# Kernel tuning notes

Measured on AMD Instinct MI355X. Metric: run time of the kernel, lower is better.

The kernel has to match this reference:

```python
import jax, jax.numpy as jnp
import numpy as np

# BatchIrregularDownsample2d(number_downsample=2) faithful JAX reference.
# The torch module does host-synced, per-batch mask-driven compaction with
# data-dependent slicing. Index arithmetic is done host-side with numpy on the
# concrete integer pooling_mask (it is a non-differentiable int constant, and the
# original module syncs it to host via .item() anyway); the heavy data movement
# (gather over [B,C,N]) is done in jnp.

D = 2                      # number_downsample
B, C, H, W = 8, 256, 256, 256
BLOCK = 2 ** D             # quadtree alignment block (4x4)


def _build_mask(seed=0):
    """Quadtree-valid mask [B,1,H,W]: each aligned 4x4 block has one level in {0,1,2};
    identical histogram per batch (static shapes), different spatial layout."""
    hb, wb = H // BLOCK, W // BLOCK
    n = hb * wb                                  # 4096 blocks
    counts = [n - 2 * (n // 3), n // 3, n // 3]  # [1366, 1365, 1365]
    base = np.repeat(np.arange(D + 1), counts)
    out = []
    for b in range(B):
        rng = np.random.RandomState(seed + b)
        v = base.copy()
        rng.shuffle(v)
        m = v.reshape(hb, wb).repeat(BLOCK, 0).repeat(BLOCK, 1)
        out.append(m)
    return np.stack(out)[:, None].astype(np.int32)


def _build_indices(mask_np):
    """Replicates the per-batch compaction of the torch module, returning a dense
    gather-index matrix G [B,M] into input's token dim and a validity mask V [B,M]
    (zeros emulate the original's zero padding to max_elements)."""
    Bm = mask_np.shape[0]
    s = 2 ** (D - 1)
    per_batch = []
    for b in range(Bm):
        m = mask_np[b, 0]
        start = 0
        for i in range(D - 1):                   # start_idx: higher-res prefix
            start += int((m == i).sum()) // 4 ** i
        cs = (m >= D - 1)[::s, ::s]              # current_scale_mask, subsampled
        dt = (m < D)[::s, ::s]                   # dont_touch_mask, subsampled
        r, c = np.nonzero(cs)                    # row-major, matches torch.nonzero
        topleft = ((r % 2) + (c % 2)) == 0       # top-left of each 2x2 pool window
        dt_at = dt[r, c]
        keep_lower = topleft & ~dt_at            # pooled-down representatives
        pos = np.arange(r.shape[0])              # rank inside graph_current_res
        idx_b = np.concatenate([
            np.arange(start),                    # graph_higher_res (untouched prefix)
            start + pos[dt_at],                  # output_dont_touch
            start + pos[keep_lower],             # output_lower_res
        ])
        per_batch.append(idx_b)
    M = max(len(x) for x in per_batch)           # max_elements across batch
    G = np.zeros((Bm, M), np.int32)
    V = np.zeros((Bm, M), np.float32)
    for b, idx_b in enumerate(per_batch):
        G[b, :len(idx_b)] = idx_b
        V[b, :len(idx_b)] = 1.0
    return jnp.asarray(G), jnp.asarray(V)


def setup_inputs() -> dict:
    mask_np = _build_mask()
    # N = max_b nr_valid_elements_current (tokens actually addressed by the slicing)
    N = 0
    for b in range(B):
        m = mask_np[b, 0]
        n = 0
        for i in range(D):
            n += int(((m == i) if i < D - 1 else (m >= i)).sum()) // 4 ** i
        N = max(N, n)
    key = jax.random.key(0)
    x = jax.random.normal(key, (B, C, N), dtype=jnp.float32)
    return {"input": x, "pooling_mask": jnp.asarray(mask_np)}


def reference(input, pooling_mask):
    G, V = _build_indices(np.asarray(pooling_mask))
    # one fused gather over the token dim + zero-padding via validity mask
    out = jnp.take_along_axis(input, G[:, None, :], axis=2) * V[:, None, :]
    return out
```

## Files before the change

kernel.cpp:

```cpp
#include <hip/hip_runtime.h>
#include <hip/hip_bf16.h>


#define HW_FULL 65536
#define T1     1024
#define PER_T  16
#define CS_CAP 11264
#define TB     512

typedef float f4a __attribute__((ext_vector_type(4), aligned(4)));
typedef float f4v __attribute__((ext_vector_type(4)));
typedef int   i4a __attribute__((ext_vector_type(4), aligned(4)));

__global__ __launch_bounds__(1024) void build_idx_kernel(
    const int* __restrict__ mask, int* __restrict__ hdr, int* __restrict__ gt, int M)
{
    const int b = blockIdx.x;
    const int t = threadIdx.x;
    const int* mb = mask + (long long)b * HW_FULL;

    unsigned char fl[PER_T];
    unsigned long long local = 0ULL;
    #pragma unroll
    for (int k = 0; k < PER_T; ++k) {
        int e = t * PER_T + k;
        int r = e >> 7;
        int c = e & 127;
        int m = mb[(r << 9) + (c << 1)];
        int z  = (m == 0);
        int cs = (m >= 1);
        int dt = (m == 1);
        int tl = ((r | c) & 1) == 0;
        int kl = (tl && (m >= 2)) ? 1 : 0;
        fl[k] = (unsigned char)(z | (cs << 1) | (dt << 2) | (kl << 3));
        local += (unsigned long long)z
               | ((unsigned long long)cs << 16)
               | ((unsigned long long)dt << 32)
               | ((unsigned long long)kl << 48);
    }

    __shared__ unsigned long long sh[T1];
    sh[t] = local;
    __syncthreads();
    for (int off = 1; off < T1; off <<= 1) {
        unsigned long long v = (t >= off) ? sh[t - off] : 0ULL;
        __syncthreads();
        sh[t] += v;
        __syncthreads();
    }
    unsigned long long tot = sh[T1 - 1];
    unsigned long long ex  = (t > 0) ? sh[t - 1] : 0ULL;

    const int zt    = (int)( tot        & 0xFFFF);
    const int cst   = (int)((tot >> 16) & 0xFFFF);
    const int ndt   = (int)((tot >> 32) & 0xFFFF);
    const int nkl   = (int)((tot >> 48) & 0xFFFF);
    const int start = zt * 4;

    int csP = (int)((ex >> 16) & 0xFFFF);
    int dtP = (int)((ex >> 32) & 0xFFFF);
    int klP = (int)((ex >> 48) & 0xFFFF);

    int* gtb = gt + (long long)b * M;
    #pragma unroll
    for (int k = 0; k < PER_T; ++k) {
        int f = fl[k];
        if (f & 4) { gtb[dtP]       = start + csP; ++dtP; }
        if (f & 8) { gtb[ndt + klP] = start + csP; ++klP; }
        if (f & 2) { ++csP; }
    }

    if (t == 0) {
        hdr[b * 4 + 0] = start;
        hdr[b * 4 + 1] = cst;
        hdr[b * 4 + 2] = ndt + nkl;
        hdr[b * 4 + 3] = start + ndt + nkl;
    }
}

__global__ __launch_bounds__(TB) void fused_row_kernel(
    const float* __restrict__ in, const int* __restrict__ hdr,
    const int* __restrict__ gt, float* __restrict__ out,
    int N, int M, int cshift)
{
    const int row   = blockIdx.x;
    const int b     = row >> cshift;
    const int start = hdr[b * 4 + 0];
    const int csn   = hdr[b * 4 + 1];
    const int ntail = hdr[b * 4 + 2];
    const long long rowM = (long long)row * M;
    const long long rowN = (long long)row * N;
    const int tid = threadIdx.x;

    const float* rin  = in  + rowN;
    const float* src  = rin + start;
    const int*   gtb  = gt + (long long)b * M;
    float*       rout = out + rowM;

    __shared__ __align__(16) float lds[CS_CAP];
    const bool staged = (csn <= CS_CAP);

    if (staged) {
        const int cs4 = csn & ~3;
        for (int i = tid << 2; i < cs4; i += (TB << 2)) {
            f4a lv = *reinterpret_cast<const f4a*>(src + i);
            f4v v; v.x = lv.x; v.y = lv.y; v.z = lv.z; v.w = lv.w;
            *reinterpret_cast<f4v*>(&lds[i]) = v;
        }
        if (tid < (csn & 3)) lds[(csn & ~3) + tid] = src[(csn & ~3) + tid];
    }

    const int h  = (int)((4 - (rowM & 3)) & 3);
    const int nq = (start >= h) ? ((start - h) >> 2) : 0;
    for (int k = tid; k < nq; k += TB) {
        const int j = h + (k << 2);
        f4a lv = *reinterpret_cast<const f4a*>(rin + j);
        f4v v; v.x = lv.x; v.y = lv.y; v.z = lv.z; v.w = lv.w;
        __builtin_nontemporal_store(v, reinterpret_cast<f4v*>(rout + j));
    }
    if (tid == 0) {
        const int hh = (h < start) ? h : start;
        for (int j = 0; j < hh; ++j)
            __builtin_nontemporal_store(rin[j], rout + j);
        if (start >= h) {
            const int base = h + (nq << 2);
            for (int j = base; j < start; ++j)
                __builtin_nontemporal_store(rin[j], rout + j);
        }
    }

    __syncthreads();

    const int span = M - start;
    const int h2   = (h < span) ? h : span;
    const int nq2  = (span >= h) ? ((span - h) >> 2) : 0;

    for (int k = tid; k < nq2; k += TB) {
        const int t = h + (k << 2);
        i4a g = *reinterpret_cast<const i4a*>(gtb + t);
        f4v v;
        v.x = (t + 0 < ntail) ? (staged ? lds[g.x - start] : rin[g.x]) : 0.0f;
        v.y = (t + 1 < ntail) ? (staged ? lds[g.y - start] : rin[g.y]) : 0.0f;
        v.z = (t + 2 < ntail) ? (staged ? lds[g.z - start] : rin[g.z]) : 0.0f;
        v.w = (t + 3 < ntail) ? (staged ? lds[g.w - start] : rin[g.w]) : 0.0f;
        __builtin_nontemporal_store(v, reinterpret_cast<f4v*>(rout + start + t));
    }
    if (tid == TB - 1) {
        for (int t = 0; t < h2; ++t) {
            float x = (t < ntail) ? (staged ? lds[gtb[t] - start] : rin[gtb[t]]) : 0.0f;
            __builtin_nontemporal_store(x, rout + start + t);
        }
        if (span >= h) {
            for (int t = h + (nq2 << 2); t < span; ++t) {
                float x = (t < ntail) ? (staged ? lds[gtb[t] - start] : rin[gtb[t]]) : 0.0f;
                __builtin_nontemporal_store(x, rout + start + t);
            }
        }
    }
}

extern "C" void kernel_launch(void* const* d_in, const int* in_sizes, int n_in,
                              void* d_out, int out_size, void* d_ws, size_t ws_size,
                              hipStream_t stream) {
    const float* x    = (const float*)d_in[0];
    const int*   mask = (const int*)d_in[1];
    float*       out  = (float*)d_out;

    const int B = in_sizes[1] / HW_FULL;
    const int C = 256;
    const int N = in_sizes[0] / (B * C);
    const int M = out_size   / (B * C);
    const int nrows = B * C;

    int cshift = 0;
    while ((1 << cshift) < C) ++cshift;

    int* hdr = (int*)d_ws;
    int* gt  = hdr + 32;

    build_idx_kernel<<<B, T1, 0, stream>>>(mask, hdr, gt, M);
    fused_row_kernel<<<nrows, TB, 0, stream>>>(x, hdr, gt, out, N, M, cshift);
}
```

Measured before the change: 101.0 us.

## Prefetch staging loads into registers and use wave-shuffle scan for index build

The index-build kernel now writes the per-element flags to shared memory with coalesced mask reads, then replaces the 1024-step shared-memory Hillis-Steele scan (with two barriers per step) by a wave-level shuffle scan followed by a 16-wide scan of wave totals. In the row kernel, the current-scale segment is loaded into up to six float4 registers per thread before the prefix copy and written to LDS afterwards, so those global loads overlap with the prefix copy traffic. The register staging covers at most 6*512*4 = 12288 elements, which exceeds CS_CAP, so the staged path stays fully covered, at the cost of higher register pressure.

```diff
diff --git a/kernel.cpp b/kernel.cpp
--- a/kernel.cpp
+++ b/kernel.cpp
@@ -3,10 +3,12 @@
 
 
 #define HW_FULL 65536
+#define SUBN   16384
 #define T1     1024
 #define PER_T  16
 #define CS_CAP 11264
 #define TB     512
+#define STI    6
 
 typedef float f4a __attribute__((ext_vector_type(4), aligned(4)));
 typedef float f4v __attribute__((ext_vector_type(4)));
@@ -19,11 +21,12 @@
     const int t = threadIdx.x;
     const int* mb = mask + (long long)b * HW_FULL;
 
-    unsigned char fl[PER_T];
-    unsigned long long local = 0ULL;
-    #pragma unroll
-    for (int k = 0; k < PER_T; ++k) {
-        int e = t * PER_T + k;
+    __shared__ unsigned char flags[SUBN];
+    __shared__ unsigned long long wsum[16];
+
+    #pragma unroll
+    for (int k = 0; k < 16; ++k) {
+        int e = (k << 10) + t;
         int r = e >> 7;
         int c = e & 127;
         int m = mb[(r << 9) + (c << 1)];
@@ -32,24 +35,45 @@
         int dt = (m == 1);
         int tl = ((r | c) & 1) == 0;
         int kl = (tl && (m >= 2)) ? 1 : 0;
-        fl[k] = (unsigned char)(z | (cs << 1) | (dt << 2) | (kl << 3));
-        local += (unsigned long long)z
-               | ((unsigned long long)cs << 16)
-               | ((unsigned long long)dt << 32)
-               | ((unsigned long long)kl << 48);
-    }
-
-    __shared__ unsigned long long sh[T1];
-    sh[t] = local;
-    __syncthreads();
-    for (int off = 1; off < T1; off <<= 1) {
-        unsigned long long v = (t >= off) ? sh[t - off] : 0ULL;
-        __syncthreads();
-        sh[t] += v;
-        __syncthreads();
-    }
-    unsigned long long tot = sh[T1 - 1];
-    unsigned long long ex  = (t > 0) ? sh[t - 1] : 0ULL;
+        flags[e] = (unsigned char)(z | (cs << 1) | (dt << 2) | (kl << 3));
+    }
+    __syncthreads();
+
+    unsigned char fl[PER_T];
+    unsigned long long local = 0ULL;
+    #pragma unroll
+    for (int k = 0; k < PER_T; ++k) {
+        unsigned char f = flags[t * PER_T + k];
+        fl[k] = f;
+        local += (unsigned long long)(f & 1)
+               | ((unsigned long long)((f >> 1) & 1) << 16)
+               | ((unsigned long long)((f >> 2) & 1) << 32)
+               | ((unsigned long long)((f >> 3) & 1) << 48);
+    }
+
+    unsigned long long v = local;
+    #pragma unroll
+    for (int off = 1; off < 64; off <<= 1) {
+        unsigned long long n = __shfl_up(v, off, 64);
+        if ((t & 63) >= off) v += n;
+    }
+    if ((t & 63) == 63) wsum[t >> 6] = v;
+    __syncthreads();
+    if (t < 16) {
+        unsigned long long w = wsum[t];
+        #pragma unroll
+        for (int off = 1; off < 16; off <<= 1) {
+            unsigned long long n = __shfl_up(w, off, 16);
+            if (t >= off) w += n;
+        }
+        wsum[t] = w;
+    }
+    __syncthreads();
+
+    unsigned long long waveoff = (t >= 64) ? wsum[(t >> 6) - 1] : 0ULL;
+    unsigned long long incl = v + waveoff;
+    unsigned long long tot  = wsum[15];
+    unsigned long long ex   = incl - local;
 
     const int zt    = (int)( tot        & 0xFFFF);
     const int cst   = (int)((tot >> 16) & 0xFFFF);
@@ -99,15 +123,15 @@
 
     __shared__ __align__(16) float lds[CS_CAP];
     const bool staged = (csn <= CS_CAP);
-
+    const int  cs4    = csn & ~3;
+
+    f4a sreg[STI];
     if (staged) {
-        const int cs4 = csn & ~3;
-        for (int i = tid << 2; i < cs4; i += (TB << 2)) {
-            f4a lv = *reinterpret_cast<const f4a*>(src + i);
-            f4v v; v.x = lv.x; v.y = lv.y; v.z = lv.z; v.w = lv.w;
-            *reinterpret_cast<f4v*>(&lds[i]) = v;
-        }
-        if (tid < (csn & 3)) lds[(csn & ~3) + tid] = src[(csn & ~3) + tid];
+        #pragma unroll
+        for (int it = 0; it < STI; ++it) {
+            const int i = (tid << 2) + it * (TB << 2);
+            if (i < cs4) sreg[it] = *reinterpret_cast<const f4a*>(src + i);
+        }
     }
 
     const int h  = (int)((4 - (rowM & 3)) & 3);
@@ -123,10 +147,22 @@
         for (int j = 0; j < hh; ++j)
             __builtin_nontemporal_store(rin[j], rout + j);
         if (start >= h) {
-            const int base = h + (nq << 2);
-            for (int j = base; j < start; ++j)
+            for (int j = h + (nq << 2); j < start; ++j)
                 __builtin_nontemporal_store(rin[j], rout + j);
         }
+    }
+
+    if (staged) {
+        #pragma unroll
+        for (int it = 0; it < STI; ++it) {
+            const int i = (tid << 2) + it * (TB << 2);
+            if (i < cs4) {
+                f4v v; v.x = sreg[it].x; v.y = sreg[it].y;
+                       v.z = sreg[it].z; v.w = sreg[it].w;
+                *reinterpret_cast<f4v*>(&lds[i]) = v;
+            }
+        }
+        if (tid < (csn & 3)) lds[cs4 + tid] = src[cs4 + tid];
     }
 
     __syncthreads();
```

Result: faster. 93.68 us (-7.3%).
